# Optimization experiments

Measured on AMD Instinct MI355X. Metric: run time of the kernel, lower is better.

The kernel has to match this reference:

```python
import jax, jax.numpy as jnp
import numpy as np

N_HEADS = 8

def setup_inputs() -> dict:
    key = jax.random.key(0)
    ks = jax.random.split(key, 5)
    d = 256
    B, N = 2, 4096
    scale = 1.0 / np.sqrt(d)
    return {
        "x_q": jax.random.normal(ks[0], (B, N, d), jnp.float32),
        "x_kv": jax.random.normal(ks[1], (B, N, d), jnp.float32),
        "Wq": jax.random.normal(ks[2], (d, d), jnp.float32) * scale,
        "bq": jnp.zeros((d,), jnp.float32),
        "Wk": jax.random.normal(ks[3], (d, d), jnp.float32) * scale,
        "bk": jnp.zeros((d,), jnp.float32),
        "Wv": jax.random.normal(ks[4], (d, d), jnp.float32) * scale,
        "bv": jnp.zeros((d,), jnp.float32),
    }


def reference(x_q, x_kv, Wq, bq, Wk, bk, Wv, bv):
    B, Nq, d = x_q.shape
    H = N_HEADS
    dh = d // H
    # linear projections (torch Linear: x @ W^T + b)
    q = x_q @ Wq.T + bq            # [B, Nq, d]
    k = x_kv @ Wk.T + bk           # [B, Nk, d]
    v = x_kv @ Wv.T + bv           # [B, Nk, d]
    # split heads -> [B, H, N, dh]
    q = q.reshape(B, Nq, H, dh).transpose(0, 2, 1, 3)
    k = k.reshape(B, -1, H, dh).transpose(0, 2, 1, 3)
    v = v.reshape(B, -1, H, dh).transpose(0, 2, 1, 3)
    # scores [B, H, Nq, Nk], softmax over keys
    scores = jnp.einsum('bhqd,bhkd->bhqk', q, k) / jnp.sqrt(jnp.asarray(dh, q.dtype))
    attn = jax.nn.softmax(scores, axis=-1)
    out = jnp.einsum('bhqk,bhkd->bhqd', attn, v)   # [B, H, Nq, dh]
    return out.transpose(0, 2, 1, 3).reshape(B, Nq, H * dh)
```

## Files before the change

kernel.cpp:

```cpp
#include <hip/hip_runtime.h>
#include <stdint.h>

#define BATCH 2
#define NSEQ 4096
#define DM 256
#define NHEAD 8
#define DH 32
#define SCALE 0.17677669529663687f

#if __has_builtin(__builtin_amdgcn_exp2f)
#define EXP2W(x) __builtin_amdgcn_exp2f(x)
#define QPRE (SCALE * 1.44269504088896340736f)
#else
#define EXP2W(x) __expf((x) * 0.69314718055994530942f)
#define QPRE (SCALE * 1.44269504088896340736f)
#endif

typedef unsigned short ushort_t;
typedef __attribute__((ext_vector_type(8))) short short8;
typedef __attribute__((ext_vector_type(4))) float float4v;

__device__ __forceinline__ ushort_t f2bf(float f) {
    union { float f; uint32_t i; } x; x.f = f;
    uint32_t i = x.i;
    i += ((i >> 16) & 1u) + 0x7fffu;
    return (ushort_t)(i >> 16);
}
__device__ __forceinline__ uint32_t rne16(float f) {
    const uint32_t i = __float_as_uint(f);
    return i + 0x7fffu + ((i >> 16) & 1u);
}
__device__ __forceinline__ uint32_t pkrne(float a, float b) {
    return __builtin_amdgcn_perm(rne16(b), rne16(a), 0x07060302u);
}

#define RST 264
__global__ __launch_bounds__(256) void proj_kernel(
    const float* __restrict__ x_q, const float* __restrict__ x_kv,
    const float* __restrict__ Wq, const float* __restrict__ bq,
    const float* __restrict__ Wk, const float* __restrict__ bk,
    const float* __restrict__ Wv, const float* __restrict__ bv,
    ushort_t* __restrict__ Qh, ushort_t* __restrict__ Kh,
    ushort_t* __restrict__ Vt)
{
    const int mat = blockIdx.y;
    const int n0  = blockIdx.x * 32;
    const float* x    = (mat == 0) ? x_q : x_kv;
    const float* W    = (mat == 0) ? Wq : (mat == 1) ? Wk : Wv;
    const float* bias = (mat == 0) ? bq : (mat == 1) ? bk : bv;

    __shared__ __align__(16) ushort_t xls[32 * RST];
    const int t = threadIdx.x;

    {
        const int r  = t >> 3;
        const int c0 = (t & 7) * 32;
        const float* src = x + (size_t)(n0 + r) * DM + c0;
        uint32_t d[16];
        #pragma unroll
        for (int i = 0; i < 8; i++) {
            float4 v = *(const float4*)(src + i * 4);
            d[i * 2]     = pkrne(v.x, v.y);
            d[i * 2 + 1] = pkrne(v.z, v.w);
        }
        uint32_t* dst = (uint32_t*)&xls[r * RST + c0];
        #pragma unroll
        for (int i = 0; i < 4; i++)
            *(uint4*)(dst + i * 4) = *(const uint4*)&d[i * 4];
    }
    __syncthreads();

    const int w    = t >> 6;
    const int l    = t & 63;
    const int lm   = l & 15;
    const int quad = l >> 4;
    const int j0   = w * 64;

    float4v acc[2][4];
    #pragma unroll
    for (int rt = 0; rt < 2; rt++)
        #pragma unroll
        for (int jt = 0; jt < 4; jt++)
            acc[rt][jt] = (float4v){0.f, 0.f, 0.f, 0.f};

    for (int kc = 0; kc < DM / 32; kc++) {
        short8 af[2];
        #pragma unroll
        for (int rt = 0; rt < 2; rt++)
            af[rt] = *(const short8*)&xls[(rt * 16 + lm) * RST + kc * 32 + quad * 8];
        #pragma unroll
        for (int jt = 0; jt < 4; jt++) {
            const float* wp = W + (size_t)(j0 + jt * 16 + lm) * DM + kc * 32 + quad * 8;
            float4 w0 = *(const float4*)wp;
            float4 w1 = *(const float4*)(wp + 4);
            uint32_t bd[4] = { pkrne(w0.x, w0.y), pkrne(w0.z, w0.w),
                               pkrne(w1.x, w1.y), pkrne(w1.z, w1.w) };
            short8 bf = *(const short8*)bd;
            acc[0][jt] = __builtin_amdgcn_mfma_f32_16x16x32_bf16(af[0], bf, acc[0][jt], 0, 0, 0);
            acc[1][jt] = __builtin_amdgcn_mfma_f32_16x16x32_bf16(af[1], bf, acc[1][jt], 0, 0, 0);
        }
    }

    const int bb = n0 >> 12;
    const int cn = n0 & (NSEQ - 1);
    #pragma unroll
    for (int jt = 0; jt < 4; jt++) {
        const int j  = j0 + jt * 16 + lm;
        const int h  = j >> 5, dd = j & 31;
        const int bh = bb * NHEAD + h;
        const float bj = bias[j];
        #pragma unroll
        for (int rt = 0; rt < 2; rt++) {
            if (mat == 2) {
                union { ushort_t u[4]; uint2 v; } pk;
                #pragma unroll
                for (int r = 0; r < 4; r++) pk.u[r] = f2bf(acc[rt][jt][r] + bj);
                *(uint2*)&Vt[((size_t)bh * DH + dd) * NSEQ + cn + quad * 8 + rt * 4] = pk.v;
            } else if (mat == 0) {
                const int nn = cn + rt * 16 + quad * 4;
                #pragma unroll
                for (int r = 0; r < 4; r++)
                    Qh[((size_t)bh * NSEQ + nn + r) * DH + dd] =
                        f2bf((acc[rt][jt][r] + bj) * QPRE);
            } else {
                const int nn = cn + rt * 16 + quad * 4;
                #pragma unroll
                for (int r = 0; r < 4; r++)
                    Kh[((size_t)bh * NSEQ + nn + r) * DH + dd] = f2bf(acc[rt][jt][r] + bj);
            }
        }
    }
}

__global__ __launch_bounds__(256) void fattn_kernel(
    const ushort_t* __restrict__ Qh, const ushort_t* __restrict__ Kh,
    const ushort_t* __restrict__ Vt, float* __restrict__ out)
{
    const int w    = threadIdx.x >> 6;
    const int l    = threadIdx.x & 63;
    const int lm   = l & 15;
    const int quad = l >> 4;
    const int qb   = blockIdx.x & 31;
    const int bh   = blockIdx.x >> 5;
    const int b    = bh >> 3, h = bh & 7;
    const int q0   = qb * 128 + w * 32;

    const ushort_t* Qb = Qh + (size_t)bh * NSEQ * DH;
    const ushort_t* Kb = Kh + (size_t)bh * NSEQ * DH;
    const ushort_t* Vb = Vt + (size_t)bh * DH * NSEQ;

    short8 qf[2];
    #pragma unroll
    for (int qt = 0; qt < 2; qt++)
        qf[qt] = *(const short8*)(Qb + (size_t)(q0 + qt * 16 + lm) * DH + quad * 8);

    short8 ones;
    #pragma unroll
    for (int i = 0; i < 8; i++) ones[i] = (short)0x3F80;

    float4v accO[2][2], accL[2];
    #pragma unroll
    for (int qt = 0; qt < 2; qt++) {
        accO[qt][0] = (float4v){0.f, 0.f, 0.f, 0.f};
        accO[qt][1] = (float4v){0.f, 0.f, 0.f, 0.f};
        accL[qt]    = (float4v){0.f, 0.f, 0.f, 0.f};
    }
    const float4v zero = {0.f, 0.f, 0.f, 0.f};

#define KLD(k, off) (*(const short8*)(Kb + (size_t)((k) + (off) + lm) * DH + quad * 8))
#define VLD(k, half) (*(const short8*)(Vb + (size_t)((half) + lm) * NSEQ + (k) + quad * 8))

    short8 kf0 = KLD(0, 0), kf1 = KLD(0, 16);
    short8 vf0 = VLD(0, 0), vf1 = VLD(0, 16);

    for (int k0 = 0; k0 < NSEQ; k0 += 32) {
        const int kn = (k0 + 32) & (NSEQ - 1);
        short8 nk0 = KLD(kn, 0), nk1 = KLD(kn, 16);
        short8 nv0 = VLD(kn, 0), nv1 = VLD(kn, 16);

        #pragma unroll
        for (int qt = 0; qt < 2; qt++) {
            float4v s0 = __builtin_amdgcn_mfma_f32_16x16x32_bf16(kf0, qf[qt], zero, 0, 0, 0);
            float4v s1 = __builtin_amdgcn_mfma_f32_16x16x32_bf16(kf1, qf[qt], zero, 0, 0, 0);
            float p0[4], p1[4];
            #pragma unroll
            for (int r = 0; r < 4; r++) {
                p0[r] = EXP2W(s0[r]);
                p1[r] = EXP2W(s1[r]);
            }
            uint32_t pd[4] = { pkrne(p0[0], p0[1]), pkrne(p0[2], p0[3]),
                               pkrne(p1[0], p1[1]), pkrne(p1[2], p1[3]) };
            short8 pf = *(const short8*)pd;
            accO[qt][0] = __builtin_amdgcn_mfma_f32_16x16x32_bf16(pf, vf0, accO[qt][0], 0, 0, 0);
            accO[qt][1] = __builtin_amdgcn_mfma_f32_16x16x32_bf16(pf, vf1, accO[qt][1], 0, 0, 0);
            accL[qt]    = __builtin_amdgcn_mfma_f32_16x16x32_bf16(pf, ones, accL[qt], 0, 0, 0);
        }

        kf0 = nk0; kf1 = nk1; vf0 = nv0; vf1 = nv1;
    }
#undef KLD
#undef VLD

    #pragma unroll
    for (int qt = 0; qt < 2; qt++)
        #pragma unroll
        for (int r = 0; r < 4; r++) {
            const float inv = 1.0f / accL[qt][r];
            const int q = q0 + qt * 16 + quad * 4 + r;
            float* orow = out + ((size_t)b * NSEQ + q) * DM + h * DH;
            orow[lm]      = accO[qt][0][r] * inv;
            orow[16 + lm] = accO[qt][1][r] * inv;
        }
}

extern "C" void kernel_launch(void* const* d_in, const int* in_sizes, int n_in,
                              void* d_out, int out_size, void* d_ws, size_t ws_size,
                              hipStream_t stream)
{
    const float* x_q  = (const float*)d_in[0];
    const float* x_kv = (const float*)d_in[1];
    const float* Wq   = (const float*)d_in[2];
    const float* bq   = (const float*)d_in[3];
    const float* Wk   = (const float*)d_in[4];
    const float* bk   = (const float*)d_in[5];
    const float* Wv   = (const float*)d_in[6];
    const float* bv   = (const float*)d_in[7];
    float* out = (float*)d_out;

    const size_t per = (size_t)BATCH * NHEAD * NSEQ * DH;
    ushort_t* Qh = (ushort_t*)d_ws;
    ushort_t* Kh = Qh + per;
    ushort_t* Vt = Kh + per;

    dim3 pgrid(BATCH * NSEQ / 32, 3);
    proj_kernel<<<pgrid, 256, 0, stream>>>(x_q, x_kv, Wq, bq, Wk, bk, Wv, bv,
                                           Qh, Kh, Vt);

    fattn_kernel<<<BATCH * NHEAD * 32, 256, 0, stream>>>(Qh, Kh, Vt, out);
}
```

Before: 190.1 us.

## Split attention keys across waves, remap blocks per XCD, use hardware bf16 pack

The attention kernel now assigns each block 32 queries and splits the 4096 keys across its four waves (1024 each). Partial outputs and row sums are combined through shared memory before a vectorized float4 store. The grid grows from 512 to 2048 blocks, and the block index is remapped so each XCD handles fixed heads for better L2 locality of K/V. The bf16 packing also switches to the hardware cvt_pk_bf16_f32 instruction when available, at the cost of an extra LDS reduction and barrier.

```diff
diff --git a/kernel.cpp b/kernel.cpp
--- a/kernel.cpp
+++ b/kernel.cpp
@@ -10,11 +10,10 @@
 
 #if __has_builtin(__builtin_amdgcn_exp2f)
 #define EXP2W(x) __builtin_amdgcn_exp2f(x)
-#define QPRE (SCALE * 1.44269504088896340736f)
 #else
 #define EXP2W(x) __expf((x) * 0.69314718055994530942f)
+#endif
 #define QPRE (SCALE * 1.44269504088896340736f)
-#endif
 
 typedef unsigned short ushort_t;
 typedef __attribute__((ext_vector_type(8))) short short8;
@@ -30,9 +29,18 @@
     const uint32_t i = __float_as_uint(f);
     return i + 0x7fffu + ((i >> 16) & 1u);
 }
-__device__ __forceinline__ uint32_t pkrne(float a, float b) {
+#if __has_builtin(__builtin_amdgcn_cvt_pk_bf16_f32)
+typedef __bf16 bf16x2_t __attribute__((ext_vector_type(2)));
+__device__ __forceinline__ uint32_t pk2(float a, float b) {
+    union { bf16x2_t v; uint32_t u; } c;
+    c.v = __builtin_amdgcn_cvt_pk_bf16_f32(a, b);
+    return c.u;
+}
+#else
+__device__ __forceinline__ uint32_t pk2(float a, float b) {
     return __builtin_amdgcn_perm(rne16(b), rne16(a), 0x07060302u);
 }
+#endif
 
 #define RST 264
 __global__ __launch_bounds__(256) void proj_kernel(
@@ -60,8 +68,8 @@
         #pragma unroll
         for (int i = 0; i < 8; i++) {
             float4 v = *(const float4*)(src + i * 4);
-            d[i * 2]     = pkrne(v.x, v.y);
-            d[i * 2 + 1] = pkrne(v.z, v.w);
+            d[i * 2]     = pk2(v.x, v.y);
+            d[i * 2 + 1] = pk2(v.z, v.w);
         }
         uint32_t* dst = (uint32_t*)&xls[r * RST + c0];
         #pragma unroll
@@ -93,8 +101,8 @@
             const float* wp = W + (size_t)(j0 + jt * 16 + lm) * DM + kc * 32 + quad * 8;
             float4 w0 = *(const float4*)wp;
             float4 w1 = *(const float4*)(wp + 4);
-            uint32_t bd[4] = { pkrne(w0.x, w0.y), pkrne(w0.z, w0.w),
-                               pkrne(w1.x, w1.y), pkrne(w1.z, w1.w) };
+            uint32_t bd[4] = { pk2(w0.x, w0.y), pk2(w0.z, w0.w),
+                               pk2(w1.x, w1.y), pk2(w1.z, w1.w) };
             short8 bf = *(const short8*)bd;
             acc[0][jt] = __builtin_amdgcn_mfma_f32_16x16x32_bf16(af[0], bf, acc[0][jt], 0, 0, 0);
             acc[1][jt] = __builtin_amdgcn_mfma_f32_16x16x32_bf16(af[1], bf, acc[1][jt], 0, 0, 0);
@@ -136,14 +144,19 @@
     const ushort_t* __restrict__ Qh, const ushort_t* __restrict__ Kh,
     const ushort_t* __restrict__ Vt, float* __restrict__ out)
 {
-    const int w    = threadIdx.x >> 6;
+    const int blk  = blockIdx.x;
+    const int xcd  = blk & 7;
+    const int idx  = blk >> 3;
+    const int bh   = xcd + 8 * (idx & 1);
+    const int qb   = idx >> 1;
+    const int q0   = qb * 32;
+    const int b    = bh >> 3, h = bh & 7;
+
+    const int wv   = threadIdx.x >> 6;
     const int l    = threadIdx.x & 63;
     const int lm   = l & 15;
     const int quad = l >> 4;
-    const int qb   = blockIdx.x & 31;
-    const int bh   = blockIdx.x >> 5;
-    const int b    = bh >> 3, h = bh & 7;
-    const int q0   = qb * 128 + w * 32;
+    const int kbase = wv * 1024;
 
     const ushort_t* Qb = Qh + (size_t)bh * NSEQ * DH;
     const ushort_t* Kb = Kh + (size_t)bh * NSEQ * DH;
@@ -170,11 +183,11 @@
 #define KLD(k, off) (*(const short8*)(Kb + (size_t)((k) + (off) + lm) * DH + quad * 8))
 #define VLD(k, half) (*(const short8*)(Vb + (size_t)((half) + lm) * NSEQ + (k) + quad * 8))
 
-    short8 kf0 = KLD(0, 0), kf1 = KLD(0, 16);
-    short8 vf0 = VLD(0, 0), vf1 = VLD(0, 16);
-
-    for (int k0 = 0; k0 < NSEQ; k0 += 32) {
-        const int kn = (k0 + 32) & (NSEQ - 1);
+    short8 kf0 = KLD(kbase, 0), kf1 = KLD(kbase, 16);
+    short8 vf0 = VLD(kbase, 0), vf1 = VLD(kbase, 16);
+
+    for (int kk = 0; kk < 1024; kk += 32) {
+        const int kn = kbase + ((kk + 32) & 1023);
         short8 nk0 = KLD(kn, 0), nk1 = KLD(kn, 16);
         short8 nv0 = VLD(kn, 0), nv1 = VLD(kn, 16);
 
@@ -188,8 +201,8 @@
                 p0[r] = EXP2W(s0[r]);
                 p1[r] = EXP2W(s1[r]);
             }
-            uint32_t pd[4] = { pkrne(p0[0], p0[1]), pkrne(p0[2], p0[3]),
-                               pkrne(p1[0], p1[1]), pkrne(p1[2], p1[3]) };
+            uint32_t pd[4] = { pk2(p0[0], p0[1]), pk2(p0[2], p0[3]),
+                               pk2(p1[0], p1[1]), pk2(p1[2], p1[3]) };
             short8 pf = *(const short8*)pd;
             accO[qt][0] = __builtin_amdgcn_mfma_f32_16x16x32_bf16(pf, vf0, accO[qt][0], 0, 0, 0);
             accO[qt][1] = __builtin_amdgcn_mfma_f32_16x16x32_bf16(pf, vf1, accO[qt][1], 0, 0, 0);
@@ -201,16 +214,37 @@
 #undef KLD
 #undef VLD
 
+    __shared__ __align__(16) float OB[4][32][36];
+    __shared__ float LB[4][32];
+
     #pragma unroll
     for (int qt = 0; qt < 2; qt++)
         #pragma unroll
         for (int r = 0; r < 4; r++) {
-            const float inv = 1.0f / accL[qt][r];
-            const int q = q0 + qt * 16 + quad * 4 + r;
-            float* orow = out + ((size_t)b * NSEQ + q) * DM + h * DH;
-            orow[lm]      = accO[qt][0][r] * inv;
-            orow[16 + lm] = accO[qt][1][r] * inv;
-        }
+            const int ql = qt * 16 + quad * 4 + r;
+            OB[wv][ql][lm]      = accO[qt][0][r];
+            OB[wv][ql][16 + lm] = accO[qt][1][r];
+            if (lm == 0) LB[wv][ql] = accL[qt][r];
+        }
+    __syncthreads();
+
+    {
+        const int t  = threadIdx.x;
+        const int ql = t >> 3;
+        const int d0 = (t & 7) * 4;
+        float4 o0 = *(const float4*)&OB[0][ql][d0];
+        float4 o1 = *(const float4*)&OB[1][ql][d0];
+        float4 o2 = *(const float4*)&OB[2][ql][d0];
+        float4 o3 = *(const float4*)&OB[3][ql][d0];
+        const float L = LB[0][ql] + LB[1][ql] + LB[2][ql] + LB[3][ql];
+        const float inv = 1.0f / L;
+        float4 res;
+        res.x = (o0.x + o1.x + o2.x + o3.x) * inv;
+        res.y = (o0.y + o1.y + o2.y + o3.y) * inv;
+        res.z = (o0.z + o1.z + o2.z + o3.z) * inv;
+        res.w = (o0.w + o1.w + o2.w + o3.w) * inv;
+        *(float4*)&out[((size_t)b * NSEQ + q0 + ql) * DM + h * DH + d0] = res;
+    }
 }
 
 extern "C" void kernel_launch(void* const* d_in, const int* in_sizes, int n_in,
@@ -236,5 +270,5 @@
     proj_kernel<<<pgrid, 256, 0, stream>>>(x_q, x_kv, Wq, bq, Wk, bk, Wv, bv,
                                            Qh, Kh, Vt);
 
-    fattn_kernel<<<BATCH * NHEAD * 32, 256, 0, stream>>>(Qh, Kh, Vt, out);
-}
+    fattn_kernel<<<2048, 256, 0, stream>>>(Qh, Kh, Vt, out);
+}
```

After: 194.3 us. 1.02x slower.
